# Kernel optimization log

Hardware: AMD Instinct MI355X
Metric: run time of the kernel (lower is better)

## Reference

```python
import jax, jax.numpy as jnp
import numpy as np

THRESH = 0.5

def setup_inputs() -> dict:
    key = jax.random.key(0)
    mask = jax.random.uniform(key, (128, 1, 512, 512), dtype=jnp.float32)
    return {"mask": mask}

def _minmax_plus1(hit, full):
    # hit: [N, L] bool. Returns (min_idx, max_idx+1); (0, full) if no hit in row.
    any_hit = jnp.any(hit, axis=1)
    lo = jnp.argmax(hit, axis=1).astype(jnp.int32)
    hi = (hit.shape[1] - jnp.argmax(hit[:, ::-1], axis=1)).astype(jnp.int32)  # last hit + 1
    lo = jnp.where(any_hit, lo, jnp.int32(0))
    hi = jnp.where(any_hit, hi, jnp.int32(full))
    return lo, hi

def reference(mask):
    # mask: [N, 1, H, W] -> bbox [N, 4] = (y_min, x_min, y_max, x_max)
    m = jnp.squeeze(mask, axis=1)            # [N, H, W]
    N, H, W = m.shape
    wmat = jnp.max(m, axis=1) >= THRESH      # [N, W] column hits
    hmat = jnp.max(m, axis=2) >= THRESH      # [N, H] row hits
    xmin, xmax = _minmax_plus1(wmat, W)
    ymin, ymax = _minmax_plus1(hmat, H)
    return jnp.stack((ymin, xmin, ymax, xmax), axis=-1)  # [N, 4] int32
```

## Files before the change

kernel.cpp:

```cpp
#include <hip/hip_runtime.h>
#include <climits>


#define THRESH 0.5f

static constexpr int N = 128;
static constexpr int H = 512;
static constexpr int W = 512;
static constexpr int G = 8;
static constexpr int ROWS = H / G;
static constexpr int BLK = 256;
static constexpr int W4 = W / 4;

__global__ __launch_bounds__(BLK)
void bbox_partial(const float* __restrict__ mask, int* __restrict__ partials) {
    const int n = blockIdx.x;
    const int g = blockIdx.y;
    const float4* base =
        (const float4*)(mask + (size_t)n * H * W + (size_t)g * ROWS * W);

    int ymin = INT_MAX, ymax = -1, xmin = INT_MAX, xmax = -1;

    #pragma unroll 4
    for (int i = threadIdx.x; i < ROWS * W4; i += BLK) {
        float4 v = base[i];
        int h = g * ROWS + (i >> 7);
        int w = (i & (W4 - 1)) << 2;
        bool b0 = v.x >= THRESH;
        bool b1 = v.y >= THRESH;
        bool b2 = v.z >= THRESH;
        bool b3 = v.w >= THRESH;
        if (b0 | b1 | b2 | b3) { ymin = min(ymin, h); ymax = max(ymax, h); }
        if (b0) { xmin = min(xmin, w + 0); xmax = max(xmax, w + 0); }
        if (b1) { xmin = min(xmin, w + 1); xmax = max(xmax, w + 1); }
        if (b2) { xmin = min(xmin, w + 2); xmax = max(xmax, w + 2); }
        if (b3) { xmin = min(xmin, w + 3); xmax = max(xmax, w + 3); }
    }

    #pragma unroll
    for (int off = 32; off > 0; off >>= 1) {
        ymin = min(ymin, __shfl_down(ymin, off, 64));
        ymax = max(ymax, __shfl_down(ymax, off, 64));
        xmin = min(xmin, __shfl_down(xmin, off, 64));
        xmax = max(xmax, __shfl_down(xmax, off, 64));
    }

    __shared__ int s[BLK / 64][4];
    const int wave = threadIdx.x >> 6;
    const int lane = threadIdx.x & 63;
    if (lane == 0) {
        s[wave][0] = ymin; s[wave][1] = ymax; s[wave][2] = xmin; s[wave][3] = xmax;
    }
    __syncthreads();
    if (threadIdx.x == 0) {
        int a = s[0][0], b = s[0][1], c = s[0][2], d = s[0][3];
        #pragma unroll
        for (int wv = 1; wv < BLK / 64; ++wv) {
            a = min(a, s[wv][0]); b = max(b, s[wv][1]);
            c = min(c, s[wv][2]); d = max(d, s[wv][3]);
        }
        int* p = partials + ((n * G + g) << 2);
        p[0] = a; p[1] = b; p[2] = c; p[3] = d;
    }
}

__global__ __launch_bounds__(128)
void bbox_final(const int* __restrict__ partials, int* __restrict__ out) {
    const int n = threadIdx.x;
    if (n >= N) return;
    int ymin = INT_MAX, ymax = -1, xmin = INT_MAX, xmax = -1;
    #pragma unroll
    for (int g = 0; g < G; ++g) {
        const int* p = partials + ((n * G + g) << 2);
        ymin = min(ymin, p[0]); ymax = max(ymax, p[1]);
        xmin = min(xmin, p[2]); xmax = max(xmax, p[3]);
    }
    int4 r;
    if (ymax < 0) {
        r = make_int4(0, 0, H, W);
    } else {
        r = make_int4(ymin, xmin, ymax + 1, xmax + 1);
    }
    ((int4*)out)[n] = r;
}

extern "C" void kernel_launch(void* const* d_in, const int* in_sizes, int n_in,
                              void* d_out, int out_size, void* d_ws, size_t ws_size,
                              hipStream_t stream) {
    const float* mask = (const float*)d_in[0];
    int* partials = (int*)d_ws;
    int* out = (int*)d_out;

    dim3 grid(N, G);
    bbox_partial<<<grid, BLK, 0, stream>>>(mask, partials);
    bbox_final<<<1, 128, 0, stream>>>(partials, out);
}
```

Measured before the change: 187.8 us.

## Fuse bbox reduction into one kernel with atomics and column-max accumulation

Replaces the two-kernel partial/final reduction with one kernel where each block atomically merges its bounds (encoded so that only atomicMax is needed), and the last-arriving block per image writes the output. Each thread now owns a fixed column group and keeps running per-lane float maxima, so the per-element x-bound tests move out of the inner loop. The grid doubles in the row direction for more parallelism. It adds two memset launches and atomic and fence traffic per block.

```diff
diff --git a/kernel.cpp b/kernel.cpp
--- a/kernel.cpp
+++ b/kernel.cpp
@@ -7,35 +7,44 @@
 static constexpr int N = 128;
 static constexpr int H = 512;
 static constexpr int W = 512;
-static constexpr int G = 8;
+static constexpr int G = 16;
 static constexpr int ROWS = H / G;
 static constexpr int BLK = 256;
 static constexpr int W4 = W / 4;
 
 __global__ __launch_bounds__(BLK)
-void bbox_partial(const float* __restrict__ mask, int* __restrict__ partials) {
+void bbox_fused(const float* __restrict__ mask, int* __restrict__ enc,
+                int* __restrict__ cnt, int* __restrict__ out) {
     const int n = blockIdx.x;
     const int g = blockIdx.y;
     const float4* base =
         (const float4*)(mask + (size_t)n * H * W + (size_t)g * ROWS * W);
 
-    int ymin = INT_MAX, ymax = -1, xmin = INT_MAX, xmax = -1;
+    const int c  = threadIdx.x & (W4 - 1);
+    const int r0 = threadIdx.x >> 7;
+
+    int ymin = INT_MAX, ymax = -1;
+    float m0 = 0.f, m1 = 0.f, m2 = 0.f, m3 = 0.f;
 
     #pragma unroll 4
-    for (int i = threadIdx.x; i < ROWS * W4; i += BLK) {
-        float4 v = base[i];
-        int h = g * ROWS + (i >> 7);
-        int w = (i & (W4 - 1)) << 2;
-        bool b0 = v.x >= THRESH;
-        bool b1 = v.y >= THRESH;
-        bool b2 = v.z >= THRESH;
-        bool b3 = v.w >= THRESH;
-        if (b0 | b1 | b2 | b3) { ymin = min(ymin, h); ymax = max(ymax, h); }
-        if (b0) { xmin = min(xmin, w + 0); xmax = max(xmax, w + 0); }
-        if (b1) { xmin = min(xmin, w + 1); xmax = max(xmax, w + 1); }
-        if (b2) { xmin = min(xmin, w + 2); xmax = max(xmax, w + 2); }
-        if (b3) { xmin = min(xmin, w + 3); xmax = max(xmax, w + 3); }
+    for (int r = r0; r < ROWS; r += 2) {
+        float4 v = base[r * W4 + c];
+        float mx = fmaxf(fmaxf(v.x, v.y), fmaxf(v.z, v.w));
+        if (mx >= THRESH) {
+            int h = g * ROWS + r;
+            ymin = min(ymin, h);
+            ymax = max(ymax, h);
+        }
+        m0 = fmaxf(m0, v.x); m1 = fmaxf(m1, v.y);
+        m2 = fmaxf(m2, v.z); m3 = fmaxf(m3, v.w);
     }
+
+    const int w = c << 2;
+    int xmin = INT_MAX, xmax = -1;
+    if (m0 >= THRESH) { xmin = w;               xmax = w;               }
+    if (m1 >= THRESH) { xmin = min(xmin, w + 1); xmax = max(xmax, w + 1); }
+    if (m2 >= THRESH) { xmin = min(xmin, w + 2); xmax = max(xmax, w + 2); }
+    if (m3 >= THRESH) { xmin = min(xmin, w + 3); xmax = max(xmax, w + 3); }
 
     #pragma unroll
     for (int off = 32; off > 0; off >>= 1) {
@@ -52,46 +61,48 @@
         s[wave][0] = ymin; s[wave][1] = ymax; s[wave][2] = xmin; s[wave][3] = xmax;
     }
     __syncthreads();
+
     if (threadIdx.x == 0) {
-        int a = s[0][0], b = s[0][1], c = s[0][2], d = s[0][3];
+        int a = s[0][0], b = s[0][1], cc = s[0][2], d = s[0][3];
         #pragma unroll
         for (int wv = 1; wv < BLK / 64; ++wv) {
-            a = min(a, s[wv][0]); b = max(b, s[wv][1]);
-            c = min(c, s[wv][2]); d = max(d, s[wv][3]);
+            a  = min(a,  s[wv][0]); b = max(b, s[wv][1]);
+            cc = min(cc, s[wv][2]); d = max(d, s[wv][3]);
         }
-        int* p = partials + ((n * G + g) << 2);
-        p[0] = a; p[1] = b; p[2] = c; p[3] = d;
+        int* e = enc + (n << 2);
+        if (b >= 0) {
+            atomicMax(&e[0], (H - 1) - a);
+            atomicMax(&e[1], b);
+            atomicMax(&e[2], (W - 1) - cc);
+            atomicMax(&e[3], d);
+        }
+        __threadfence();
+        int old = atomicAdd(&cnt[n], 1);
+        if (old == G - 1) {
+            __threadfence();
+            int e0 = atomicMax(&e[0], -1);
+            int e1 = atomicMax(&e[1], -1);
+            int e2 = atomicMax(&e[2], -1);
+            int e3 = atomicMax(&e[3], -1);
+            int4 r;
+            if (e1 < 0) r = make_int4(0, 0, H, W);
+            else        r = make_int4((H - 1) - e0, (W - 1) - e2, e1 + 1, e3 + 1);
+            ((int4*)out)[n] = r;
+        }
     }
-}
-
-__global__ __launch_bounds__(128)
-void bbox_final(const int* __restrict__ partials, int* __restrict__ out) {
-    const int n = threadIdx.x;
-    if (n >= N) return;
-    int ymin = INT_MAX, ymax = -1, xmin = INT_MAX, xmax = -1;
-    #pragma unroll
-    for (int g = 0; g < G; ++g) {
-        const int* p = partials + ((n * G + g) << 2);
-        ymin = min(ymin, p[0]); ymax = max(ymax, p[1]);
-        xmin = min(xmin, p[2]); xmax = max(xmax, p[3]);
-    }
-    int4 r;
-    if (ymax < 0) {
-        r = make_int4(0, 0, H, W);
-    } else {
-        r = make_int4(ymin, xmin, ymax + 1, xmax + 1);
-    }
-    ((int4*)out)[n] = r;
 }
 
 extern "C" void kernel_launch(void* const* d_in, const int* in_sizes, int n_in,
                               void* d_out, int out_size, void* d_ws, size_t ws_size,
                               hipStream_t stream) {
     const float* mask = (const float*)d_in[0];
-    int* partials = (int*)d_ws;
+    int* enc = (int*)d_ws;
+    int* cnt = (int*)((char*)d_ws + N * 4 * 4);
     int* out = (int*)d_out;
 
+    hipMemsetAsync(enc, 0xFF, N * 4 * sizeof(int), stream);
+    hipMemsetAsync(cnt, 0x00, N * sizeof(int), stream);
+
     dim3 grid(N, G);
-    bbox_partial<<<grid, BLK, 0, stream>>>(mask, partials);
-    bbox_final<<<1, 128, 0, stream>>>(partials, out);
+    bbox_fused<<<grid, BLK, 0, stream>>>(mask, enc, cnt, out);
 }
```

After: 284.0 us. 1.51x slower.

## Accumulate per-thread column max, fully unroll loads, and double the row-group grid

Applied to the files above, without the earlier changes.

Each thread now always handles the same four columns, so it keeps a running float max per column and only converts to x-bounds once after the loop, rather than doing min/max index updates on every element. The loop is fully unrolled and issues four float4 loads per step to keep more memory requests in flight. Row bounds come from a per-vector max test. The grid doubles to 16 row groups per image to raise parallelism, at the cost of more partials for the final kernel to reduce.

```diff
diff --git a/kernel.cpp b/kernel.cpp
--- a/kernel.cpp
+++ b/kernel.cpp
@@ -7,10 +7,11 @@
 static constexpr int N = 128;
 static constexpr int H = 512;
 static constexpr int W = 512;
-static constexpr int G = 8;
+static constexpr int G = 16;
 static constexpr int ROWS = H / G;
 static constexpr int BLK = 256;
 static constexpr int W4 = W / 4;
+static constexpr int ITER = ROWS * W4 / BLK;
 
 __global__ __launch_bounds__(BLK)
 void bbox_partial(const float* __restrict__ mask, int* __restrict__ partials) {
@@ -19,23 +20,44 @@
     const float4* base =
         (const float4*)(mask + (size_t)n * H * W + (size_t)g * ROWS * W);
 
-    int ymin = INT_MAX, ymax = -1, xmin = INT_MAX, xmax = -1;
+    const int c  = threadIdx.x & (W4 - 1);
+    const int rb = threadIdx.x >> 7;
 
-    #pragma unroll 4
-    for (int i = threadIdx.x; i < ROWS * W4; i += BLK) {
-        float4 v = base[i];
-        int h = g * ROWS + (i >> 7);
-        int w = (i & (W4 - 1)) << 2;
-        bool b0 = v.x >= THRESH;
-        bool b1 = v.y >= THRESH;
-        bool b2 = v.z >= THRESH;
-        bool b3 = v.w >= THRESH;
-        if (b0 | b1 | b2 | b3) { ymin = min(ymin, h); ymax = max(ymax, h); }
-        if (b0) { xmin = min(xmin, w + 0); xmax = max(xmax, w + 0); }
-        if (b1) { xmin = min(xmin, w + 1); xmax = max(xmax, w + 1); }
-        if (b2) { xmin = min(xmin, w + 2); xmax = max(xmax, w + 2); }
-        if (b3) { xmin = min(xmin, w + 3); xmax = max(xmax, w + 3); }
+    int ymin = INT_MAX, ymax = -1;
+    float m0 = 0.f, m1 = 0.f, m2 = 0.f, m3 = 0.f;
+
+    #pragma unroll
+    for (int k = 0; k < ITER; k += 4) {
+        float4 v0 = base[threadIdx.x + (k + 0) * BLK];
+        float4 v1 = base[threadIdx.x + (k + 1) * BLK];
+        float4 v2 = base[threadIdx.x + (k + 2) * BLK];
+        float4 v3 = base[threadIdx.x + (k + 3) * BLK];
+
+        float x0 = fmaxf(fmaxf(v0.x, v0.y), fmaxf(v0.z, v0.w));
+        float x1 = fmaxf(fmaxf(v1.x, v1.y), fmaxf(v1.z, v1.w));
+        float x2 = fmaxf(fmaxf(v2.x, v2.y), fmaxf(v2.z, v2.w));
+        float x3 = fmaxf(fmaxf(v3.x, v3.y), fmaxf(v3.z, v3.w));
+
+        int r = 2 * k + rb;
+        if (x0 >= THRESH) { ymin = min(ymin, r + 0); ymax = max(ymax, r + 0); }
+        if (x1 >= THRESH) { ymin = min(ymin, r + 2); ymax = max(ymax, r + 2); }
+        if (x2 >= THRESH) { ymin = min(ymin, r + 4); ymax = max(ymax, r + 4); }
+        if (x3 >= THRESH) { ymin = min(ymin, r + 6); ymax = max(ymax, r + 6); }
+
+        m0 = fmaxf(fmaxf(m0, v0.x), fmaxf(v1.x, fmaxf(v2.x, v3.x)));
+        m1 = fmaxf(fmaxf(m1, v0.y), fmaxf(v1.y, fmaxf(v2.y, v3.y)));
+        m2 = fmaxf(fmaxf(m2, v0.z), fmaxf(v1.z, fmaxf(v2.z, v3.z)));
+        m3 = fmaxf(fmaxf(m3, v0.w), fmaxf(v1.w, fmaxf(v2.w, v3.w)));
     }
+
+    if (ymax >= 0) { ymin += g * ROWS; ymax += g * ROWS; }
+
+    const int w = c << 2;
+    int xmin = INT_MAX, xmax = -1;
+    if (m0 >= THRESH) { xmin = w;                xmax = w;                }
+    if (m1 >= THRESH) { xmin = min(xmin, w + 1); xmax = max(xmax, w + 1); }
+    if (m2 >= THRESH) { xmin = min(xmin, w + 2); xmax = max(xmax, w + 2); }
+    if (m3 >= THRESH) { xmin = min(xmin, w + 3); xmax = max(xmax, w + 3); }
 
     #pragma unroll
     for (int off = 32; off > 0; off >>= 1) {
@@ -53,14 +75,13 @@
     }
     __syncthreads();
     if (threadIdx.x == 0) {
-        int a = s[0][0], b = s[0][1], c = s[0][2], d = s[0][3];
+        int a = s[0][0], b = s[0][1], cc = s[0][2], d = s[0][3];
         #pragma unroll
         for (int wv = 1; wv < BLK / 64; ++wv) {
-            a = min(a, s[wv][0]); b = max(b, s[wv][1]);
-            c = min(c, s[wv][2]); d = max(d, s[wv][3]);
+            a  = min(a,  s[wv][0]); b = max(b, s[wv][1]);
+            cc = min(cc, s[wv][2]); d = max(d, s[wv][3]);
         }
-        int* p = partials + ((n * G + g) << 2);
-        p[0] = a; p[1] = b; p[2] = c; p[3] = d;
+        ((int4*)partials)[n * G + g] = make_int4(a, b, cc, d);
     }
 }
 
@@ -69,18 +90,16 @@
     const int n = threadIdx.x;
     if (n >= N) return;
     int ymin = INT_MAX, ymax = -1, xmin = INT_MAX, xmax = -1;
+    const int4* p = (const int4*)partials + n * G;
     #pragma unroll
     for (int g = 0; g < G; ++g) {
-        const int* p = partials + ((n * G + g) << 2);
-        ymin = min(ymin, p[0]); ymax = max(ymax, p[1]);
-        xmin = min(xmin, p[2]); xmax = max(xmax, p[3]);
+        int4 q = p[g];
+        ymin = min(ymin, q.x); ymax = max(ymax, q.y);
+        xmin = min(xmin, q.z); xmax = max(xmax, q.w);
     }
     int4 r;
-    if (ymax < 0) {
-        r = make_int4(0, 0, H, W);
-    } else {
-        r = make_int4(ymin, xmin, ymax + 1, xmax + 1);
-    }
+    if (ymax < 0) r = make_int4(0, 0, H, W);
+    else          r = make_int4(ymin, xmin, ymax + 1, xmax + 1);
     ((int4*)out)[n] = r;
 }
 
```

Result: no change. 189.4 us (+0.9%).
